# Kernel tuning notes

Hardware: AMD Instinct MI355X
Metric: run time of the kernel (lower is better)

The kernel has to match this reference:

```python
import jax, jax.numpy as jnp
import numpy as np

N_NODES = 100000
N_EDGES = 3200000
IN_FEATS = 512
EDGE_FEATS = 24
OUT_FEATS = 512
LN_EPS = 1e-5


def setup_inputs() -> dict:
    key = jax.random.key(0)
    ks = jax.random.split(key, 8)
    h = jax.random.normal(ks[0], (N_NODES, IN_FEATS), dtype=jnp.float32)
    m = jax.random.normal(ks[1], (N_EDGES, EDGE_FEATS), dtype=jnp.float32)
    dst = jax.random.randint(ks[2], (N_EDGES,), 0, N_NODES, dtype=jnp.int32)
    norm = jax.random.uniform(ks[3], (N_NODES, 1), dtype=jnp.float32)
    stdv = 1.0 / np.sqrt(IN_FEATS + EDGE_FEATS)
    W = jax.random.uniform(ks[4], (OUT_FEATS, IN_FEATS + EDGE_FEATS), dtype=jnp.float32, minval=-stdv, maxval=stdv)
    b = jax.random.uniform(ks[5], (OUT_FEATS,), dtype=jnp.float32, minval=-stdv, maxval=stdv)
    gamma = jnp.ones((OUT_FEATS,), dtype=jnp.float32)
    beta = jnp.zeros((OUT_FEATS,), dtype=jnp.float32)
    return {"h": h, "m": m, "dst": dst, "norm": norm, "W": W, "b": b, "gamma": gamma, "beta": beta}


def reference(h, m, dst, norm, W, b, gamma, beta):
    # copy_e + sum: segment-sum edge features into destination nodes -> [N, 24]
    ah = jax.ops.segment_sum(m, dst, num_segments=N_NODES)
    # scale by per-node norm, concat with node features -> [N, in+24]
    x = jnp.concatenate([h, ah * norm], axis=1)
    # linear
    y = jnp.einsum('nd,od->no', x, W) + b
    # layernorm (elementwise affine)
    mu = jnp.mean(y, axis=-1, keepdims=True)
    var = jnp.mean((y - mu) ** 2, axis=-1, keepdims=True)
    y = gamma * (y - mu) * jax.lax.rsqrt(var + LN_EPS) + beta
    # activation = relu
    return jax.nn.relu(y)
```

## Files before the change

kernel.cpp:

```cpp
#include <hip/hip_runtime.h>
#include <hip/hip_bf16.h>
#include <stdint.h>

#define NN 100000
#define NE 3200000
#define EF 24
#define KF 536
#define BM 64

typedef __attribute__((ext_vector_type(8))) short bf16x8;
typedef __attribute__((ext_vector_type(4))) float f32x4;

__device__ __forceinline__ unsigned short f2bf(float f) {
  union { float f; unsigned int u; } v; v.f = f;
  unsigned int r = v.u + 0x7FFFu + ((v.u >> 16) & 1u);
  return (unsigned short)(r >> 16);
}

__device__ __forceinline__ void gload_lds16(const void* g, void* l) {
  __builtin_amdgcn_global_load_lds(
      (const __attribute__((address_space(1))) unsigned int*)g,
      (__attribute__((address_space(3))) unsigned int*)l, 16, 0, 0);
}

__global__ void wconv_kernel(const float* __restrict__ W, unsigned short* __restrict__ Wb) {
  int i = blockIdx.x * blockDim.x + threadIdx.x;
  if (i >= 17 * 32 * 64 * 8) return;
  int j = i & 7;
  int lane = (i >> 3) & 63;
  int nt = (i >> 9) & 31;
  int kt = i >> 14;
  int row = nt * 16 + (lane & 15);
  int k = kt * 32 + (lane >> 4) * 8 + j;
  float v = (k < KF) ? W[row * KF + k] : 0.0f;
  Wb[i] = f2bf(v);
}

__global__ __launch_bounds__(256) void scatter_pk_kernel(
    const float* __restrict__ m, const int* __restrict__ dst,
    unsigned int* __restrict__ acc, int base) {
  int i = base + blockIdx.x * 256 + threadIdx.x;
  if (i >= NE * 12) return;
  int e = i / 12;
  int fp = i - e * 12;
  float2 v = *(const float2*)(m + (size_t)e * EF + fp * 2);
  unsigned int pk = ((unsigned int)f2bf(v.y) << 16) | (unsigned int)f2bf(v.x);
  unsigned int* p = acc + (size_t)dst[e] * 12 + fp;
  asm volatile("global_atomic_pk_add_bf16 %0, %1, off" :: "v"(p), "v"(pk) : "memory");
}

__global__ __launch_bounds__(256) void reduce_pk_kernel(
    const unsigned int* __restrict__ acc, const float* __restrict__ norm,
    float* __restrict__ ah) {
  int i = blockIdx.x * 256 + threadIdx.x;
  if (i >= NN * 12) return;
  int n = i / 12;
  unsigned int pk = acc[i];
  float nv = norm[n];
  union { unsigned int u; float f; } lo, hi;
  lo.u = (pk & 0xFFFFu) << 16;
  hi.u = pk & 0xFFFF0000u;
  *(float2*)(ah + (size_t)i * 2) = make_float2(lo.f * nv, hi.f * nv);
}

__global__ __launch_bounds__(512, 4) void gemm_ln_kernel(
    const float* __restrict__ h, const float* __restrict__ ah,
    const unsigned short* __restrict__ Wb,
    const float* __restrict__ bias, const float* __restrict__ gamma,
    const float* __restrict__ beta, float* __restrict__ out) {
  __shared__ __align__(16) unsigned short Alds[4 * 4 * 16 * 8];
  __shared__ __align__(16) unsigned short Blds[32 * 4 * 16 * 8];
  __shared__ float red[4][BM][2];
  __shared__ float stats[BM][2];

  const int t = threadIdx.x;
  const int lane = t & 63;
  const int w = t >> 6;
  const int lgrp = lane >> 4;
  const int llow = lane & 15;
  const int mg = w >> 2;
  const int ng = w & 3;
  const int blockRow = blockIdx.x * BM;

  const int am = t >> 3;
  const int akg = (t >> 1) & 3;
  const int ahalf = t & 1;
  const int arow = blockRow + am;
  char* aldsdst = (char*)Alds + (((am >> 4) * 64 + akg * 16 + (am & 15)) * 16 + ahalf * 8);

  f32x4 acc[2][8];
#pragma unroll
  for (int i = 0; i < 2; ++i)
#pragma unroll
    for (int j = 0; j < 8; ++j) acc[i][j] = (f32x4){0.f, 0.f, 0.f, 0.f};

  float4 ra = make_float4(0.f, 0.f, 0.f, 0.f);
  if (arow < NN) ra = *(const float4*)(h + (size_t)arow * 512 + akg * 8 + ahalf * 4);

  for (int kt = 0; kt < 17; ++kt) {
    {
      const unsigned short* src = Wb + ((size_t)(kt * 32 + w) * 64 + lane) * 8;
#pragma unroll
      for (int j = 0; j < 4; ++j)
        gload_lds16(src + (size_t)j * 8 * 64 * 8, (char*)Blds + (j * 8 + w) * 1024);
    }
    {
      ushort4 bv;
      bv.x = f2bf(ra.x); bv.y = f2bf(ra.y); bv.z = f2bf(ra.z); bv.w = f2bf(ra.w);
      *(ushort4*)aldsdst = bv;
    }
    ra = make_float4(0.f, 0.f, 0.f, 0.f);
    if (kt < 16 && arow < NN) {
      if (kt < 15) {
        ra = *(const float4*)(h + (size_t)arow * 512 + (kt + 1) * 32 + akg * 8 + ahalf * 4);
      } else if (akg < 3) {
        ra = *(const float4*)(ah + (size_t)arow * EF + akg * 8 + ahalf * 4);
      }
    }
    __syncthreads();

    bf16x8 af0 = *(const bf16x8*)((const char*)Alds + (((mg * 2 + 0) * 64) + lane) * 16);
    bf16x8 af1 = *(const bf16x8*)((const char*)Alds + (((mg * 2 + 1) * 64) + lane) * 16);
#pragma unroll
    for (int j = 0; j < 8; ++j) {
      int nt = ng * 8 + j;
      bf16x8 bf = *(const bf16x8*)((const char*)Blds + ((nt * 64) + lane) * 16);
      acc[0][j] = __builtin_amdgcn_mfma_f32_16x16x32_bf16(af0, bf, acc[0][j], 0, 0, 0);
      acc[1][j] = __builtin_amdgcn_mfma_f32_16x16x32_bf16(af1, bf, acc[1][j], 0, 0, 0);
    }
    __syncthreads();
  }

  float bcol[8], gcol[8], btcol[8];
#pragma unroll
  for (int j = 0; j < 8; ++j) {
    int col = (ng * 8 + j) * 16 + llow;
    bcol[j] = bias[col];
    gcol[j] = gamma[col];
    btcol[j] = beta[col];
  }
  float s[2][4], ss[2][4];
#pragma unroll
  for (int mt = 0; mt < 2; ++mt)
#pragma unroll
    for (int r = 0; r < 4; ++r) { s[mt][r] = 0.f; ss[mt][r] = 0.f; }
#pragma unroll
  for (int mt = 0; mt < 2; ++mt)
#pragma unroll
    for (int j = 0; j < 8; ++j)
#pragma unroll
      for (int r = 0; r < 4; ++r) {
        float v = acc[mt][j][r] + bcol[j];
        acc[mt][j][r] = v;
        s[mt][r] += v;
        ss[mt][r] += v * v;
      }
#pragma unroll
  for (int off = 1; off < 16; off <<= 1) {
#pragma unroll
    for (int mt = 0; mt < 2; ++mt)
#pragma unroll
      for (int r = 0; r < 4; ++r) {
        s[mt][r] += __shfl_xor(s[mt][r], off, 64);
        ss[mt][r] += __shfl_xor(ss[mt][r], off, 64);
      }
  }
  if (llow == 0) {
#pragma unroll
    for (int mt = 0; mt < 2; ++mt)
#pragma unroll
      for (int r = 0; r < 4; ++r) {
        int lrow = (mg * 2 + mt) * 16 + lgrp * 4 + r;
        red[ng][lrow][0] = s[mt][r];
        red[ng][lrow][1] = ss[mt][r];
      }
  }
  __syncthreads();
  if (t < BM) {
    float sum = red[0][t][0] + red[1][t][0] + red[2][t][0] + red[3][t][0];
    float sq = red[0][t][1] + red[1][t][1] + red[2][t][1] + red[3][t][1];
    float mean = sum * (1.0f / 512.0f);
    float var = sq * (1.0f / 512.0f) - mean * mean;
    stats[t][0] = mean;
    stats[t][1] = rsqrtf(var + 1e-5f);
  }
  __syncthreads();
#pragma unroll
  for (int mt = 0; mt < 2; ++mt) {
#pragma unroll
    for (int r = 0; r < 4; ++r) {
      int lrow = (mg * 2 + mt) * 16 + lgrp * 4 + r;
      int grow = blockRow + lrow;
      if (grow < NN) {
        float mean = stats[lrow][0];
        float rstd = stats[lrow][1];
#pragma unroll
        for (int j = 0; j < 8; ++j) {
          int col = (ng * 8 + j) * 16 + llow;
          float v = (acc[mt][j][r] - mean) * rstd * gcol[j] + btcol[j];
          out[grow * 512 + col] = fmaxf(v, 0.0f);
        }
      }
    }
  }
}

extern "C" void kernel_launch(void* const* d_in, const int* in_sizes, int n_in,
                              void* d_out, int out_size, void* d_ws, size_t ws_size,
                              hipStream_t stream) {
  const float* h = (const float*)d_in[0];
  const float* m = (const float*)d_in[1];
  const int* dst = (const int*)d_in[2];
  const float* norm = (const float*)d_in[3];
  const float* W = (const float*)d_in[4];
  const float* b = (const float*)d_in[5];
  const float* gamma = (const float*)d_in[6];
  const float* beta = (const float*)d_in[7];
  float* out = (float*)d_out;

  float* ah = (float*)d_ws;
  unsigned short* Wb = (unsigned short*)((char*)d_ws + 9600000);

  unsigned int* acc = (unsigned int*)d_out;

  const int HALF = NE * 12 / 2;

  hipMemsetAsync(acc, 0, (size_t)NN * 12 * sizeof(unsigned int), stream);
  wconv_kernel<<<(17 * 32 * 64 * 8 + 255) / 256, 256, 0, stream>>>(W, Wb);
  scatter_pk_kernel<<<HALF / 256, 256, 0, stream>>>(m, dst, acc, 0);
  scatter_pk_kernel<<<HALF / 256, 256, 0, stream>>>(m, dst, acc, HALF);
  reduce_pk_kernel<<<(NN * 12 + 255) / 256, 256, 0, stream>>>(acc, norm, ah);
  gemm_ln_kernel<<<(NN + BM - 1) / BM, 512, 0, stream>>>(h, ah, Wb, b, gamma, beta, out);
}
```

Before: 418.5 us.

## Load GEMM operands directly into registers, drop LDS staging and barriers

The GEMM kernel no longer stages A and B tiles through shared memory. Each wave now loads its own h rows and pre-swizzled weight fragments straight from global memory into registers and converts A with packed bf16 conversion instructions. This removes the two barriers per k-step and the LDS traffic, but each wave now fetches B redundantly and the loads are not overlapped through explicit double buffering. The scatter is also merged into a single launch.

```diff
diff --git a/kernel.cpp b/kernel.cpp
--- a/kernel.cpp
+++ b/kernel.cpp
@@ -17,10 +17,10 @@
   return (unsigned short)(r >> 16);
 }
 
-__device__ __forceinline__ void gload_lds16(const void* g, void* l) {
-  __builtin_amdgcn_global_load_lds(
-      (const __attribute__((address_space(1))) unsigned int*)g,
-      (__attribute__((address_space(3))) unsigned int*)l, 16, 0, 0);
+__device__ __forceinline__ unsigned int cvtpk(float a, float b) {
+  unsigned int r;
+  asm("v_cvt_pk_bf16_f32 %0, %1, %2" : "=v"(r) : "v"(a), "v"(b));
+  return r;
 }
 
 __global__ void wconv_kernel(const float* __restrict__ W, unsigned short* __restrict__ Wb) {
@@ -38,8 +38,8 @@
 
 __global__ __launch_bounds__(256) void scatter_pk_kernel(
     const float* __restrict__ m, const int* __restrict__ dst,
-    unsigned int* __restrict__ acc, int base) {
-  int i = base + blockIdx.x * 256 + threadIdx.x;
+    unsigned int* __restrict__ acc) {
+  int i = blockIdx.x * 256 + threadIdx.x;
   if (i >= NE * 12) return;
   int e = i / 12;
   int fp = i - e * 12;
@@ -68,8 +68,6 @@
     const unsigned short* __restrict__ Wb,
     const float* __restrict__ bias, const float* __restrict__ gamma,
     const float* __restrict__ beta, float* __restrict__ out) {
-  __shared__ __align__(16) unsigned short Alds[4 * 4 * 16 * 8];
-  __shared__ __align__(16) unsigned short Blds[32 * 4 * 16 * 8];
   __shared__ float red[4][BM][2];
   __shared__ float stats[BM][2];
 
@@ -82,11 +80,13 @@
   const int ng = w & 3;
   const int blockRow = blockIdx.x * BM;
 
-  const int am = t >> 3;
-  const int akg = (t >> 1) & 3;
-  const int ahalf = t & 1;
-  const int arow = blockRow + am;
-  char* aldsdst = (char*)Alds + (((am >> 4) * 64 + akg * 16 + (am & 15)) * 16 + ahalf * 8);
+  int row0 = blockRow + (mg * 2 + 0) * 16 + llow;
+  int row1 = blockRow + (mg * 2 + 1) * 16 + llow;
+  if (row0 > NN - 1) row0 = NN - 1;
+  if (row1 > NN - 1) row1 = NN - 1;
+  const float* hp0 = h + (size_t)row0 * 512 + lgrp * 8;
+  const float* hp1 = h + (size_t)row1 * 512 + lgrp * 8;
+  const unsigned short* bp = Wb + ((size_t)(ng * 8) * 64 + lane) * 8;
 
   f32x4 acc[2][8];
 #pragma unroll
@@ -94,41 +94,51 @@
 #pragma unroll
     for (int j = 0; j < 8; ++j) acc[i][j] = (f32x4){0.f, 0.f, 0.f, 0.f};
 
-  float4 ra = make_float4(0.f, 0.f, 0.f, 0.f);
-  if (arow < NN) ra = *(const float4*)(h + (size_t)arow * 512 + akg * 8 + ahalf * 4);
-
-  for (int kt = 0; kt < 17; ++kt) {
-    {
-      const unsigned short* src = Wb + ((size_t)(kt * 32 + w) * 64 + lane) * 8;
-#pragma unroll
-      for (int j = 0; j < 4; ++j)
-        gload_lds16(src + (size_t)j * 8 * 64 * 8, (char*)Blds + (j * 8 + w) * 1024);
-    }
-    {
-      ushort4 bv;
-      bv.x = f2bf(ra.x); bv.y = f2bf(ra.y); bv.z = f2bf(ra.z); bv.w = f2bf(ra.w);
-      *(ushort4*)aldsdst = bv;
-    }
-    ra = make_float4(0.f, 0.f, 0.f, 0.f);
-    if (kt < 16 && arow < NN) {
-      if (kt < 15) {
-        ra = *(const float4*)(h + (size_t)arow * 512 + (kt + 1) * 32 + akg * 8 + ahalf * 4);
-      } else if (akg < 3) {
-        ra = *(const float4*)(ah + (size_t)arow * EF + akg * 8 + ahalf * 4);
-      }
-    }
-    __syncthreads();
-
-    bf16x8 af0 = *(const bf16x8*)((const char*)Alds + (((mg * 2 + 0) * 64) + lane) * 16);
-    bf16x8 af1 = *(const bf16x8*)((const char*)Alds + (((mg * 2 + 1) * 64) + lane) * 16);
+  union bfu { bf16x8 v; unsigned int u[4]; };
+
+  for (int kt = 0; kt < 16; ++kt) {
+    bf16x8 bf[8];
+#pragma unroll
+    for (int j = 0; j < 8; ++j)
+      bf[j] = *(const bf16x8*)(bp + ((size_t)(kt * 32 + j) * 64) * 8);
+    float4 a00 = *(const float4*)(hp0 + kt * 32);
+    float4 a01 = *(const float4*)(hp0 + kt * 32 + 4);
+    float4 a10 = *(const float4*)(hp1 + kt * 32);
+    float4 a11 = *(const float4*)(hp1 + kt * 32 + 4);
+    bfu af0, af1;
+    af0.u[0] = cvtpk(a00.x, a00.y); af0.u[1] = cvtpk(a00.z, a00.w);
+    af0.u[2] = cvtpk(a01.x, a01.y); af0.u[3] = cvtpk(a01.z, a01.w);
+    af1.u[0] = cvtpk(a10.x, a10.y); af1.u[1] = cvtpk(a10.z, a10.w);
+    af1.u[2] = cvtpk(a11.x, a11.y); af1.u[3] = cvtpk(a11.z, a11.w);
 #pragma unroll
     for (int j = 0; j < 8; ++j) {
-      int nt = ng * 8 + j;
-      bf16x8 bf = *(const bf16x8*)((const char*)Blds + ((nt * 64) + lane) * 16);
-      acc[0][j] = __builtin_amdgcn_mfma_f32_16x16x32_bf16(af0, bf, acc[0][j], 0, 0, 0);
-      acc[1][j] = __builtin_amdgcn_mfma_f32_16x16x32_bf16(af1, bf, acc[1][j], 0, 0, 0);
-    }
-    __syncthreads();
+      acc[0][j] = __builtin_amdgcn_mfma_f32_16x16x32_bf16(af0.v, bf[j], acc[0][j], 0, 0, 0);
+      acc[1][j] = __builtin_amdgcn_mfma_f32_16x16x32_bf16(af1.v, bf[j], acc[1][j], 0, 0, 0);
+    }
+  }
+  {
+    bf16x8 bf[8];
+#pragma unroll
+    for (int j = 0; j < 8; ++j)
+      bf[j] = *(const bf16x8*)(bp + ((size_t)(16 * 32 + j) * 64) * 8);
+    float4 a00, a01, a10, a11;
+    a00 = a01 = a10 = a11 = make_float4(0.f, 0.f, 0.f, 0.f);
+    if (lgrp < 3) {
+      a00 = *(const float4*)(ah + (size_t)row0 * EF + lgrp * 8);
+      a01 = *(const float4*)(ah + (size_t)row0 * EF + lgrp * 8 + 4);
+      a10 = *(const float4*)(ah + (size_t)row1 * EF + lgrp * 8);
+      a11 = *(const float4*)(ah + (size_t)row1 * EF + lgrp * 8 + 4);
+    }
+    bfu af0, af1;
+    af0.u[0] = cvtpk(a00.x, a00.y); af0.u[1] = cvtpk(a00.z, a00.w);
+    af0.u[2] = cvtpk(a01.x, a01.y); af0.u[3] = cvtpk(a01.z, a01.w);
+    af1.u[0] = cvtpk(a10.x, a10.y); af1.u[1] = cvtpk(a10.z, a10.w);
+    af1.u[2] = cvtpk(a11.x, a11.y); af1.u[3] = cvtpk(a11.z, a11.w);
+#pragma unroll
+    for (int j = 0; j < 8; ++j) {
+      acc[0][j] = __builtin_amdgcn_mfma_f32_16x16x32_bf16(af0.v, bf[j], acc[0][j], 0, 0, 0);
+      acc[1][j] = __builtin_amdgcn_mfma_f32_16x16x32_bf16(af1.v, bf[j], acc[1][j], 0, 0, 0);
+    }
   }
 
   float bcol[8], gcol[8], btcol[8];
@@ -223,12 +233,9 @@
 
   unsigned int* acc = (unsigned int*)d_out;
 
-  const int HALF = NE * 12 / 2;
-
   hipMemsetAsync(acc, 0, (size_t)NN * 12 * sizeof(unsigned int), stream);
   wconv_kernel<<<(17 * 32 * 64 * 8 + 255) / 256, 256, 0, stream>>>(W, Wb);
-  scatter_pk_kernel<<<HALF / 256, 256, 0, stream>>>(m, dst, acc, 0);
-  scatter_pk_kernel<<<HALF / 256, 256, 0, stream>>>(m, dst, acc, HALF);
+  scatter_pk_kernel<<<(NE * 12 + 255) / 256, 256, 0, stream>>>(m, dst, acc);
   reduce_pk_kernel<<<(NN * 12 + 255) / 256, 256, 0, stream>>>(acc, norm, ah);
   gemm_ln_kernel<<<(NN + BM - 1) / BM, 512, 0, stream>>>(h, ah, Wb, b, gamma, beta, out);
 }
```

Result: slower. 500.0 us (+19.5%).
